# Kernel tuning notes

Hardware: AMD Instinct MI355X
Metric: run time of the kernel (lower is better)

The kernel has to match this reference:

```python
import jax, jax.numpy as jnp
import numpy as np

# pywt db4 decomposition filters (8 taps)
DEC_LO = np.array([-0.010597401784997278, 0.032883011666982945, 0.030841381835986965,
                   -0.18703481171888114, -0.02798376941698385, 0.6308807679295904,
                   0.7148465705525415, 0.23037781330885523], dtype=np.float32)
DEC_HI = np.array([-0.23037781330885523, 0.7148465705525415, -0.6308807679295904,
                   -0.02798376941698385, 0.18703481171888114, 0.030841381835986965,
                   -0.032883011666982945, -0.010597401784997278], dtype=np.float32)
LEVEL = 6
F = 8  # filter length

# pywt dwt with mode='zero' is exactly full_convolve(x, filt)[1::2].
# We realize it as a strided correlation with the flipped filters:
# out[i] = sum_j x_pad[2i+j] * filt[F-1-j], x padded left by F-2 zeros.
_KERNEL = jnp.asarray(np.stack([DEC_LO[::-1], DEC_HI[::-1]])[:, None, :])  # [2,1,F]

def _dwt_step(x):
    # x: [B, N] -> (cA [B, M], cD [B, M]) with M = floor((N+F-1)/2)
    N = x.shape[-1]
    M = (N + F - 1) // 2
    xp = jnp.pad(x, ((0, 0), (F - 2, F)))[:, None, :]          # [B,1,Npad]
    y = jax.lax.conv_general_dilated(
        xp, _KERNEL.astype(x.dtype), window_strides=(2,), padding='VALID',
        dimension_numbers=('NCH', 'OIH', 'NCH'))                # [B,2,>=M]
    return y[:, 0, :M], y[:, 1, :M]


def setup_inputs() -> dict:
    key = jax.random.key(0)
    x = jax.random.normal(key, (64, 262144), dtype=jnp.float32)
    return {"x": x}


def reference(x):
    # Cascaded 6-level db4 DWT, zero boundary mode.
    a = x
    details = []  # finest first
    for _ in range(LEVEL):
        a, d = _dwt_step(a)
        details.append(d)
    # Match torch module: details[0] = coarsest detail (pywt coeffs[1])
    return (a,) + tuple(details[::-1])
```

## Files before the change

### kernel.cpp

```cpp
#include <hip/hip_runtime.h>


#define NT 256

#define N0 262144
#define M1 131075
#define M2 65541
#define M3 32774
#define M4 16390
#define M5 8198
#define M6 4102
#define WSTRIDE 65544

#define OFF_A6 ((size_t)0)
#define OFF_D6 ((size_t)262528)
#define OFF_D5 ((size_t)525056)
#define OFF_D4 ((size_t)1049728)
#define OFF_D3 ((size_t)2098688)
#define OFF_D2 ((size_t)4196224)
#define OFF_D1 ((size_t)8390848)

typedef float f4_t __attribute__((ext_vector_type(4)));
typedef f4_t f4u_t __attribute__((aligned(4)));

__device__ __constant__ float RLO[8] = {
    0.23037781330885523f, 0.7148465705525415f, 0.6308807679295904f,
    -0.02798376941698385f, -0.18703481171888114f, 0.030841381835986965f,
    0.032883011666982945f, -0.010597401784997278f};
__device__ __constant__ float RHI[8] = {
    -0.010597401784997278f, -0.032883011666982945f, 0.030841381835986965f,
    0.18703481171888114f, -0.02798376941698385f, -0.6308807679295904f,
    0.7148465705525415f, -0.23037781330885523f};

template <int NC, int SLO, int SHI, int SHIFT, bool A_GLOBAL, bool A_NT>
__device__ __forceinline__ void level_fast(const f4_t* __restrict__ sE4,
                                           const f4_t* __restrict__ sO4,
                                           float2* __restrict__ dE2,
                                           float2* __restrict__ dO2,
                                           float* __restrict__ gA,
                                           float* __restrict__ gD) {
  for (int c = threadIdx.x; c < NC; c += NT) {
    f4_t e0 = sE4[c], e1 = sE4[c + 1];
    f4_t o0 = sO4[c], o1 = sO4[c + 1];
    float e[8] = {e0.x, e0.y, e0.z, e0.w, e1.x, e1.y, e1.z, e1.w};
    float o[8] = {o0.x, o0.y, o0.z, o0.w, o1.x, o1.y, o1.z, o1.w};
    float a[4], d[4];
#pragma unroll
    for (int j = 0; j < 4; ++j) {
      float aa = 0.f, dd = 0.f;
#pragma unroll
      for (int t = 0; t < 4; ++t) {
        float ev = e[j + t + SHIFT], ov = o[j + t + SHIFT];
        aa = fmaf(RLO[2 * t], ev, aa);
        aa = fmaf(RLO[2 * t + 1], ov, aa);
        dd = fmaf(RHI[2 * t], ev, dd);
        dd = fmaf(RHI[2 * t + 1], ov, dd);
      }
      a[j] = aa;
      d[j] = dd;
    }
    if (A_GLOBAL) {
      f4_t av = {a[0], a[1], a[2], a[3]};
      if (A_NT)
        __builtin_nontemporal_store(av, (f4u_t*)(gA + 4 * c));
      else
        *(f4u_t*)(gA + 4 * c) = av;
    } else {
      dE2[c] = make_float2(a[0], a[2]);
      dO2[c] = make_float2(a[1], a[3]);
    }
    const int l0 = 4 * c;
    const int lo = l0 < SLO ? SLO : l0;
    const int hi = (l0 + 4) < SHI ? (l0 + 4) : SHI;
    if (lo == l0 && hi == l0 + 4) {
      f4_t dv = {d[0], d[1], d[2], d[3]};
      __builtin_nontemporal_store(dv, (f4u_t*)(gD + l0));
    } else {
      for (int j = lo - l0; j < hi - l0; ++j)
        __builtin_nontemporal_store(d[j], gD + l0 + j);
    }
  }
}

__global__ __launch_bounds__(NT, 8) void dwt_k1(const float* __restrict__ x,
                                                float* __restrict__ out,
                                                float* __restrict__ ws) {
  const int q = blockIdx.x;
  const int row = blockIdx.y;
  const int tid = threadIdx.x;
  __shared__ float lds[3112];

  const int b2 = q << 9;
  const int b1h = (q << 10) - 6;
  const int b0h = (q << 11) - 18;

  float* gD1 = out + OFF_D1 + (size_t)row * M1 + b1h;
  float* gD2 = out + OFF_D2 + (size_t)row * M2 + b2;
  float* gA2 = ws + (size_t)row * WSTRIDE + b2;

  if (q >= 1 && q <= 127) {
    const f4_t* __restrict__ xs4 =
        (const f4_t*)(x + (size_t)row * N0 + (b0h - 2));
    float2* Ep2 = (float2*)(lds + 0);
    float2* Op2 = (float2*)(lds + 1036);
    for (int m = tid; m < 517; m += NT) {
      f4_t v = xs4[m];
      Ep2[m] = make_float2(v.x, v.z);
      Op2[m] = make_float2(v.y, v.w);
    }
    __syncthreads();
    level_fast<258, 6, 1030, 1, false, false>(
        (const f4_t*)(lds + 0), (const f4_t*)(lds + 1036),
        (float2*)(lds + 2072), (float2*)(lds + 2592), nullptr, gD1);
    __syncthreads();
    level_fast<128, 0, 512, 0, true, false>(
        (const f4_t*)(lds + 2072), (const f4_t*)(lds + 2592), nullptr, nullptr,
        gA2, gD2);
  } else {
    float* xf = lds;
    float* a1 = lds + 2072;
    const float* __restrict__ xr = x + (size_t)row * N0;
    for (int l = tid; l < 2072; l += NT) {
      int g = b0h + l;
      xf[l] = (g >= 0 && g < N0) ? xr[g] : 0.f;
    }
    __syncthreads();
    const int own0 = q << 10;
    for (int lA = tid; lA < 1032; lA += NT) {
      int g = b1h + lA;
      float aa = 0.f, dd = 0.f;
      if (g >= 0 && g < M1) {
#pragma unroll
        for (int m = 0; m < 8; ++m) {
          float v = xf[2 * lA + m];
          aa = fmaf(RLO[m], v, aa);
          dd = fmaf(RHI[m], v, dd);
        }
      }
      a1[lA] = aa;
      if (g >= own0 && g < own0 + 1024 && g < M1)
        __builtin_nontemporal_store(dd, gD1 + lA);
    }
    __syncthreads();
    for (int l = tid; l < 512; l += NT) {
      int g2 = b2 + l;
      if (g2 < M2) {
        float aa = 0.f, dd = 0.f;
#pragma unroll
        for (int m = 0; m < 8; ++m) {
          float v = a1[2 * l + m];
          aa = fmaf(RLO[m], v, aa);
          dd = fmaf(RHI[m], v, dd);
        }
        __builtin_nontemporal_store(dd, gD2 + l);
        gA2[l] = aa;
      }
    }
  }
}

__global__ __launch_bounds__(NT, 8) void dwt_k2(const float* __restrict__ ws,
                                                float* __restrict__ out) {
  const int p = blockIdx.x;
  const int row = blockIdx.y;
  const int tid = threadIdx.x;
  __shared__ float lds[1680];

  const int b6 = p << 6;
  const int b5 = (p << 7) - 6;
  const int b4 = (p << 8) - 18;
  const int b3 = (p << 9) - 42;
  const int b2t = (p << 10) - 90;

  float* gD3 = out + OFF_D3 + (size_t)row * M3 + b3;
  float* gD4 = out + OFF_D4 + (size_t)row * M4 + b4;
  float* gD5 = out + OFF_D5 + (size_t)row * M5 + b5;
  float* gD6 = out + OFF_D6 + (size_t)row * M6 + b6;
  float* gA6 = out + OFF_A6 + (size_t)row * M6 + b6;
  const float* __restrict__ wr = ws + (size_t)row * WSTRIDE;

  if (p >= 1 && p <= 63) {
    const f4_t* __restrict__ s4 = (const f4_t*)(wr + (b2t - 2));
    float2* Ep2 = (float2*)(lds + 0);
    float2* Op2 = (float2*)(lds + 560);
    for (int m = tid; m < 279; m += NT) {
      f4_t v = s4[m];
      Ep2[m] = make_float2(v.x, v.z);
      Op2[m] = make_float2(v.y, v.w);
    }
    __syncthreads();
    level_fast<139, 0, 554, 1, false, false>(
        (const f4_t*)(lds + 0), (const f4_t*)(lds + 560),
        (float2*)(lds + 1120), (float2*)(lds + 1400), nullptr, gD3);
    __syncthreads();
    level_fast<69, 0, 274, 0, false, false>(
        (const f4_t*)(lds + 1120), (const f4_t*)(lds + 1400),
        (float2*)(lds + 0), (float2*)(lds + 560), nullptr, gD4);
    __syncthreads();
    level_fast<34, 0, 134, 0, false, false>(
        (const f4_t*)(lds + 0), (const f4_t*)(lds + 560),
        (float2*)(lds + 1120), (float2*)(lds + 1400), nullptr, gD5);
    __syncthreads();
    level_fast<16, 0, 64, 0, true, true>(
        (const f4_t*)(lds + 1120), (const f4_t*)(lds + 1400), nullptr, nullptr,
        gA6, gD6);
  } else {
    float* xf = lds;
    float* bb = lds + 1120;
    for (int l = tid; l < 1116; l += NT) {
      int g = b2t + l;
      xf[l] = (g >= 0 && g < M2) ? wr[g] : 0.f;
    }
    __syncthreads();
    for (int l = tid; l < 554; l += NT) {
      int g = b3 + l;
      float aa = 0.f, dd = 0.f;
      if (g >= 0 && g < M3) {
#pragma unroll
        for (int m = 0; m < 8; ++m) {
          float v = xf[2 * l + m];
          aa = fmaf(RLO[m], v, aa);
          dd = fmaf(RHI[m], v, dd);
        }
      }
      bb[l] = aa;
      if (l >= 42 && g < M3) __builtin_nontemporal_store(dd, gD3 + l);
    }
    __syncthreads();
    for (int l = tid; l < 274; l += NT) {
      int g = b4 + l;
      float aa = 0.f, dd = 0.f;
      if (g >= 0 && g < M4) {
#pragma unroll
        for (int m = 0; m < 8; ++m) {
          float v = bb[2 * l + m];
          aa = fmaf(RLO[m], v, aa);
          dd = fmaf(RHI[m], v, dd);
        }
      }
      lds[l] = aa;
      if (l >= 18 && g < M4) __builtin_nontemporal_store(dd, gD4 + l);
    }
    __syncthreads();
    for (int l = tid; l < 134; l += NT) {
      int g = b5 + l;
      float aa = 0.f, dd = 0.f;
      if (g >= 0 && g < M5) {
#pragma unroll
        for (int m = 0; m < 8; ++m) {
          float v = lds[2 * l + m];
          aa = fmaf(RLO[m], v, aa);
          dd = fmaf(RHI[m], v, dd);
        }
      }
      bb[l] = aa;
      if (l >= 6 && g < M5) __builtin_nontemporal_store(dd, gD5 + l);
    }
    __syncthreads();
    for (int l = tid; l < 64; l += NT) {
      int g = b6 + l;
      if (g < M6) {
        float aa = 0.f, dd = 0.f;
#pragma unroll
        for (int m = 0; m < 8; ++m) {
          float v = bb[2 * l + m];
          aa = fmaf(RLO[m], v, aa);
          dd = fmaf(RHI[m], v, dd);
        }
        __builtin_nontemporal_store(aa, gA6 + l);
        __builtin_nontemporal_store(dd, gD6 + l);
      }
    }
  }
}

extern "C" void kernel_launch(void* const* d_in, const int* in_sizes, int n_in,
                              void* d_out, int out_size, void* d_ws,
                              size_t ws_size, hipStream_t stream) {
  const float* x = (const float*)d_in[0];
  float* out = (float*)d_out;
  float* ws = (float*)d_ws;
  dwt_k1<<<dim3(129, 64), NT, 0, stream>>>(x, out, ws);
  dwt_k2<<<dim3(65, 64), NT, 0, stream>>>(ws, out);
}
```

Baseline: 123.2 us.

## Fuse levels 1-2 in registers per thread with smaller tiles in first kernel

```diff
diff --git a/kernel.cpp b/kernel.cpp
--- a/kernel.cpp
+++ b/kernel.cpp
@@ -1,7 +1,8 @@
 #include <hip/hip_runtime.h>
 
 
-#define NT 256
+#define NT1 128
+#define NT2 256
 
 #define N0 262144
 #define M1 131075
@@ -22,6 +23,8 @@
 
 typedef float f4_t __attribute__((ext_vector_type(4)));
 typedef f4_t f4u_t __attribute__((aligned(4)));
+typedef float f2_t __attribute__((ext_vector_type(2)));
+typedef f2_t f2u_t __attribute__((aligned(4)));
 
 __device__ __constant__ float RLO[8] = {
     0.23037781330885523f, 0.7148465705525415f, 0.6308807679295904f,
@@ -32,6 +35,119 @@
     0.18703481171888114f, -0.02798376941698385f, -0.6308807679295904f,
     0.7148465705525415f, -0.23037781330885523f};
 
+__global__ __launch_bounds__(NT1, 6) void dwt_k1(const float* __restrict__ x,
+                                                 float* __restrict__ out,
+                                                 float* __restrict__ ws) {
+  const int q = blockIdx.x;
+  const int row = blockIdx.y;
+  const int tid = threadIdx.x;
+  __shared__ __align__(16) float lds[1600];
+
+  const int sb = (q << 10) - 20;
+  float* __restrict__ gD1 = out + OFF_D1 + (size_t)row * M1;
+  float* __restrict__ gD2 = out + OFF_D2 + (size_t)row * M2;
+  float* __restrict__ gA2 = ws + (size_t)row * WSTRIDE;
+
+  if (q >= 1 && q <= 255) {
+    const f4_t* __restrict__ xs4 = (const f4_t*)(x + (size_t)row * N0 + sb);
+    float2* E2 = (float2*)(lds);
+    float2* O2 = (float2*)(lds + 528);
+    for (int m = tid; m < 261; m += NT1) {
+      f4_t v = xs4[m];
+      E2[m] = make_float2(v.x, v.z);
+      O2[m] = make_float2(v.y, v.w);
+    }
+    __syncthreads();
+
+    const int c = tid;
+    const f4_t* E4 = (const f4_t*)(lds);
+    const f4_t* O4 = (const f4_t*)(lds + 528);
+    f4_t ea = E4[c], eb = E4[c + 1], ec = E4[c + 2], ed = E4[c + 3];
+    f4_t oa = O4[c], ob = O4[c + 1], oc = O4[c + 2], od = O4[c + 3];
+    float e[13] = {ea.y, ea.z, ea.w, eb.x, eb.y, eb.z, eb.w,
+                   ec.x, ec.y, ec.z, ec.w, ed.x, ed.y};
+    float o[13] = {oa.y, oa.z, oa.w, ob.x, ob.y, ob.z, ob.w,
+                   oc.x, oc.y, oc.z, oc.w, od.x, od.y};
+
+    float A1[10];
+#pragma unroll
+    for (int i = 0; i < 10; ++i) {
+      float aa = 0.f;
+#pragma unroll
+      for (int t = 0; t < 4; ++t) {
+        aa = fmaf(RLO[2 * t], e[i + t], aa);
+        aa = fmaf(RLO[2 * t + 1], o[i + t], aa);
+      }
+      A1[i] = aa;
+    }
+    f4_t d1v;
+#pragma unroll
+    for (int j = 0; j < 4; ++j) {
+      float dd = 0.f;
+#pragma unroll
+      for (int t = 0; t < 4; ++t) {
+        dd = fmaf(RHI[2 * t], e[j + 6 + t], dd);
+        dd = fmaf(RHI[2 * t + 1], o[j + 6 + t], dd);
+      }
+      d1v[j] = dd;
+    }
+    __builtin_nontemporal_store(d1v, (f4u_t*)(gD1 + ((q << 9) + 4 * c)));
+
+    f2_t a2v, d2v;
+#pragma unroll
+    for (int j = 0; j < 2; ++j) {
+      float aa = 0.f, dd = 0.f;
+#pragma unroll
+      for (int m = 0; m < 8; ++m) {
+        aa = fmaf(RLO[m], A1[2 * j + m], aa);
+        dd = fmaf(RHI[m], A1[2 * j + m], dd);
+      }
+      a2v[j] = aa;
+      d2v[j] = dd;
+    }
+    const int g2 = (q << 8) + 2 * c;
+    __builtin_nontemporal_store(d2v, (f2u_t*)(gD2 + g2));
+    *(f2_t*)(gA2 + g2) = a2v;
+  } else {
+    float* xf = lds;
+    float* a1 = lds + 1056;
+    const float* __restrict__ xr = x + (size_t)row * N0;
+    for (int l = tid; l < 1044; l += NT1) {
+      int g = sb + l;
+      xf[l] = (g >= 0 && g < N0) ? xr[g] : 0.f;
+    }
+    __syncthreads();
+    const int b1e = (q << 9) - 6;
+    for (int l = tid; l < 518; l += NT1) {
+      float aa = 0.f, dd = 0.f;
+#pragma unroll
+      for (int m = 0; m < 8; ++m) {
+        float v = xf[2 * l + 2 + m];
+        aa = fmaf(RLO[m], v, aa);
+        dd = fmaf(RHI[m], v, dd);
+      }
+      a1[l] = aa;
+      int h = b1e + l;
+      if (l >= 6 && h < M1) __builtin_nontemporal_store(dd, gD1 + h);
+    }
+    __syncthreads();
+    for (int l2 = tid; l2 < 256; l2 += NT1) {
+      int g2 = (q << 8) + l2;
+      if (g2 < M2) {
+        float aa = 0.f, dd = 0.f;
+#pragma unroll
+        for (int m = 0; m < 8; ++m) {
+          float v = a1[2 * l2 + m];
+          aa = fmaf(RLO[m], v, aa);
+          dd = fmaf(RHI[m], v, dd);
+        }
+        __builtin_nontemporal_store(dd, gD2 + g2);
+        gA2[g2] = aa;
+      }
+    }
+  }
+}
+
 template <int NC, int SLO, int SHI, int SHIFT, bool A_GLOBAL, bool A_NT>
 __device__ __forceinline__ void level_fast(const f4_t* __restrict__ sE4,
                                            const f4_t* __restrict__ sO4,
@@ -39,7 +155,7 @@
                                            float2* __restrict__ dO2,
                                            float* __restrict__ gA,
                                            float* __restrict__ gD) {
-  for (int c = threadIdx.x; c < NC; c += NT) {
+  for (int c = threadIdx.x; c < NC; c += NT2) {
     f4_t e0 = sE4[c], e1 = sE4[c + 1];
     f4_t o0 = sO4[c], o1 = sO4[c + 1];
     float e[8] = {e0.x, e0.y, e0.z, e0.w, e1.x, e1.y, e1.z, e1.w};
@@ -82,89 +198,12 @@
   }
 }
 
-__global__ __launch_bounds__(NT, 8) void dwt_k1(const float* __restrict__ x,
-                                                float* __restrict__ out,
-                                                float* __restrict__ ws) {
-  const int q = blockIdx.x;
-  const int row = blockIdx.y;
-  const int tid = threadIdx.x;
-  __shared__ float lds[3112];
-
-  const int b2 = q << 9;
-  const int b1h = (q << 10) - 6;
-  const int b0h = (q << 11) - 18;
-
-  float* gD1 = out + OFF_D1 + (size_t)row * M1 + b1h;
-  float* gD2 = out + OFF_D2 + (size_t)row * M2 + b2;
-  float* gA2 = ws + (size_t)row * WSTRIDE + b2;
-
-  if (q >= 1 && q <= 127) {
-    const f4_t* __restrict__ xs4 =
-        (const f4_t*)(x + (size_t)row * N0 + (b0h - 2));
-    float2* Ep2 = (float2*)(lds + 0);
-    float2* Op2 = (float2*)(lds + 1036);
-    for (int m = tid; m < 517; m += NT) {
-      f4_t v = xs4[m];
-      Ep2[m] = make_float2(v.x, v.z);
-      Op2[m] = make_float2(v.y, v.w);
-    }
-    __syncthreads();
-    level_fast<258, 6, 1030, 1, false, false>(
-        (const f4_t*)(lds + 0), (const f4_t*)(lds + 1036),
-        (float2*)(lds + 2072), (float2*)(lds + 2592), nullptr, gD1);
-    __syncthreads();
-    level_fast<128, 0, 512, 0, true, false>(
-        (const f4_t*)(lds + 2072), (const f4_t*)(lds + 2592), nullptr, nullptr,
-        gA2, gD2);
-  } else {
-    float* xf = lds;
-    float* a1 = lds + 2072;
-    const float* __restrict__ xr = x + (size_t)row * N0;
-    for (int l = tid; l < 2072; l += NT) {
-      int g = b0h + l;
-      xf[l] = (g >= 0 && g < N0) ? xr[g] : 0.f;
-    }
-    __syncthreads();
-    const int own0 = q << 10;
-    for (int lA = tid; lA < 1032; lA += NT) {
-      int g = b1h + lA;
-      float aa = 0.f, dd = 0.f;
-      if (g >= 0 && g < M1) {
-#pragma unroll
-        for (int m = 0; m < 8; ++m) {
-          float v = xf[2 * lA + m];
-          aa = fmaf(RLO[m], v, aa);
-          dd = fmaf(RHI[m], v, dd);
-        }
-      }
-      a1[lA] = aa;
-      if (g >= own0 && g < own0 + 1024 && g < M1)
-        __builtin_nontemporal_store(dd, gD1 + lA);
-    }
-    __syncthreads();
-    for (int l = tid; l < 512; l += NT) {
-      int g2 = b2 + l;
-      if (g2 < M2) {
-        float aa = 0.f, dd = 0.f;
-#pragma unroll
-        for (int m = 0; m < 8; ++m) {
-          float v = a1[2 * l + m];
-          aa = fmaf(RLO[m], v, aa);
-          dd = fmaf(RHI[m], v, dd);
-        }
-        __builtin_nontemporal_store(dd, gD2 + l);
-        gA2[l] = aa;
-      }
-    }
-  }
-}
-
-__global__ __launch_bounds__(NT, 8) void dwt_k2(const float* __restrict__ ws,
-                                                float* __restrict__ out) {
+__global__ __launch_bounds__(NT2, 8) void dwt_k2(const float* __restrict__ ws,
+                                                 float* __restrict__ out) {
   const int p = blockIdx.x;
   const int row = blockIdx.y;
   const int tid = threadIdx.x;
-  __shared__ float lds[1680];
+  __shared__ __align__(16) float lds[1680];
 
   const int b6 = p << 6;
   const int b5 = (p << 7) - 6;
@@ -183,7 +222,7 @@
     const f4_t* __restrict__ s4 = (const f4_t*)(wr + (b2t - 2));
     float2* Ep2 = (float2*)(lds + 0);
     float2* Op2 = (float2*)(lds + 560);
-    for (int m = tid; m < 279; m += NT) {
+    for (int m = tid; m < 279; m += NT2) {
       f4_t v = s4[m];
       Ep2[m] = make_float2(v.x, v.z);
       Op2[m] = make_float2(v.y, v.w);
@@ -207,12 +246,12 @@
   } else {
     float* xf = lds;
     float* bb = lds + 1120;
-    for (int l = tid; l < 1116; l += NT) {
+    for (int l = tid; l < 1116; l += NT2) {
       int g = b2t + l;
       xf[l] = (g >= 0 && g < M2) ? wr[g] : 0.f;
     }
     __syncthreads();
-    for (int l = tid; l < 554; l += NT) {
+    for (int l = tid; l < 554; l += NT2) {
       int g = b3 + l;
       float aa = 0.f, dd = 0.f;
       if (g >= 0 && g < M3) {
@@ -227,7 +266,7 @@
       if (l >= 42 && g < M3) __builtin_nontemporal_store(dd, gD3 + l);
     }
     __syncthreads();
-    for (int l = tid; l < 274; l += NT) {
+    for (int l = tid; l < 274; l += NT2) {
       int g = b4 + l;
       float aa = 0.f, dd = 0.f;
       if (g >= 0 && g < M4) {
@@ -242,7 +281,7 @@
       if (l >= 18 && g < M4) __builtin_nontemporal_store(dd, gD4 + l);
     }
     __syncthreads();
-    for (int l = tid; l < 134; l += NT) {
+    for (int l = tid; l < 134; l += NT2) {
       int g = b5 + l;
       float aa = 0.f, dd = 0.f;
       if (g >= 0 && g < M5) {
@@ -257,7 +296,7 @@
       if (l >= 6 && g < M5) __builtin_nontemporal_store(dd, gD5 + l);
     }
     __syncthreads();
-    for (int l = tid; l < 64; l += NT) {
+    for (int l = tid; l < 64; l += NT2) {
       int g = b6 + l;
       if (g < M6) {
         float aa = 0.f, dd = 0.f;
@@ -280,6 +319,6 @@
   const float* x = (const float*)d_in[0];
   float* out = (float*)d_out;
   float* ws = (float*)d_ws;
-  dwt_k1<<<dim3(129, 64), NT, 0, stream>>>(x, out, ws);
-  dwt_k2<<<dim3(65, 64), NT, 0, stream>>>(ws, out);
+  dwt_k1<<<dim3(257, 64), NT1, 0, stream>>>(x, out, ws);
+  dwt_k2<<<dim3(65, 64), NT2, 0, stream>>>(ws, out);
 }
```

Result: slower. 125.8 us (+2.2%).
